# Optimization experiments

Hardware: AMD Instinct MI355X
Metric: run time of the kernel (lower is better)

## Reference

```python
import jax, jax.numpy as jnp
import numpy as np

N, IN_DIM, HID, E = 2048, 128, 64, 32768
EPS = 1e-5  # torch BatchNorm1d / LayerNorm default eps


def setup_inputs() -> dict:
    key = jax.random.key(0)
    ks = jax.random.split(key, 12)
    s = 0.05
    return {
        "h": jax.random.normal(ks[0], (N, IN_DIM), jnp.float32),
        "local": jax.random.normal(ks[1], (N, IN_DIM), jnp.float32),
        "e": jax.random.normal(ks[2], (E, HID), jnp.float32),
        "src": jax.random.randint(ks[3], (E,), 0, N, jnp.int32),
        "dst": jax.random.randint(ks[4], (E,), 0, N, jnp.int32),
        "ln_w": jnp.ones((IN_DIM,), jnp.float32),
        "ln_b": jnp.zeros((IN_DIM,), jnp.float32),
        "conv_w": jax.random.normal(ks[5], (1, 2, 3), jnp.float32) * 0.3,
        "conv_b": jnp.zeros((1,), jnp.float32),
        "W1": jax.random.normal(ks[6], (IN_DIM, HID * HID), jnp.float32) * s,
        "b1": jnp.zeros((HID * HID,), jnp.float32),
        "Wp2": jax.random.normal(ks[7], (IN_DIM, HID), jnp.float32) * s,
        "bp2": jnp.zeros((HID,), jnp.float32),
        "W2": jax.random.normal(ks[8], (IN_DIM, HID), jnp.float32) * s,
        "b2": jnp.zeros((HID,), jnp.float32),
        "W3": jax.random.normal(ks[9], (HID, HID), jnp.float32) * s,
        "b3": jnp.zeros((HID,), jnp.float32),
        "bng_g": jnp.ones((HID,), jnp.float32),
        "bng_b": jnp.zeros((HID,), jnp.float32),
        "bnG_g": jnp.ones((HID,), jnp.float32),
        "bnG_b": jnp.zeros((HID,), jnp.float32),
        "bnL_g": jnp.ones((HID,), jnp.float32),
        "bnL_b": jnp.zeros((HID,), jnp.float32),
    }


def _bn_eval(x, g, b):
    # BatchNorm1d in eval mode, running_mean=0, running_var=1
    return x * (g / jnp.sqrt(1.0 + EPS)) + b


def _layernorm(x, w, b):
    mu = jnp.mean(x, axis=-1, keepdims=True)
    var = jnp.var(x, axis=-1, keepdims=True)
    return (x - mu) / jnp.sqrt(var + EPS) * w + b


def reference(h, local, e, src, dst, ln_w, ln_b, conv_w, conv_b,
              W1, b1, Wp2, bp2, W2, b2, W3, b3,
              bng_g, bng_b, bnG_g, bnG_b, bnL_g, bnL_b):
    # ---- local edge branch ----
    edge = jnp.stack([local[src], local[dst]], axis=1)  # [E, 2, in_dim]
    edge = _layernorm(edge, ln_w, ln_b)
    # Conv1d(2 -> 1, k=3, pad=1) over the in_dim axis
    lr_local = jax.lax.conv_general_dilated(
        edge, conv_w, window_strides=(1,), padding=[(1, 1)],
        dimension_numbers=("NCH", "OIH", "NCH"))[:, 0, :] + conv_b  # [E, in_dim]
    lr_local = jax.nn.relu(lr_local)  # dropout is identity in eval
    lr_local = lr_local @ W2 + b2  # [E, hid]

    # ---- global edge branch ----
    p1 = jax.nn.relu(h @ W1 + b1).reshape(h.shape[0], HID, HID)  # [N, hid(d), hid(k)]
    p2 = jax.nn.relu(h @ Wp2 + bp2)  # [N, hid(k)]
    # mm[i, j, d] = sum_k p1[i, d, k] * p2[j, k]; gather only needed edges
    lr_global = jnp.einsum("edk,ek->ed", p1[src], p2[dst])  # [E, hid]
    lr_global = _bn_eval(lr_global, bng_g, bng_b) @ W3 + b3
    lr_global = jax.nn.relu(_bn_eval(lr_global, bnG_g, bnG_b))

    lr_local = jax.nn.relu(_bn_eval(lr_local, bnL_g, bnL_b))
    return lr_local + lr_global + e
```

## Files before the change

kernel.cpp:

```cpp
#include <hip/hip_runtime.h>

#define N_NODES 2048
#define IN_DIM 128
#define HID 64
#define N_EDGES 32768
#define EPS 1e-5f
#define MAX_TILES 4608

typedef short short8 __attribute__((ext_vector_type(8)));
typedef float f32x4 __attribute__((ext_vector_type(4)));

__device__ __forceinline__ float relu_f(float x) { return fmaxf(x, 0.f); }

__device__ __forceinline__ unsigned short f2bf(float f) {
  unsigned int u = __float_as_uint(f);
  u = (u + 0x7fffu + ((u >> 16) & 1u)) >> 16;
  return (unsigned short)u;
}
__device__ __forceinline__ float bf2f(unsigned short h) {
  return __uint_as_float(((unsigned int)h) << 16);
}
__device__ __forceinline__ short8 pack8(const float* f) {
  short8 o;
  #pragma unroll
  for (int i = 0; i < 8; ++i) o[i] = (short)f2bf(f[i]);
  return o;
}

__global__ __launch_bounds__(256) void prep_hist(
    const float* __restrict__ h, const float* __restrict__ local,
    const float* __restrict__ ln_w, const float* __restrict__ ln_b,
    const float* __restrict__ Wp2, const float* __restrict__ bp2,
    const float* __restrict__ W1, const float* __restrict__ W2,
    const float* __restrict__ W3, const int* __restrict__ src,
    unsigned short* __restrict__ hb, unsigned short* __restrict__ lnlb,
    unsigned short* __restrict__ p2b, unsigned short* __restrict__ w1t,
    unsigned short* __restrict__ w2tb, unsigned short* __restrict__ w3tb,
    int* __restrict__ cnt, int* __restrict__ perm_padded)
{
  __shared__ __align__(16) union {
    struct { float tile[IN_DIM][65]; } tr;
    struct { float hs[4][IN_DIM]; } p2s;
  } S;
  const int b = blockIdx.x, t = threadIdx.x;
  const int w = t >> 6, l = t & 63;

  if (b < 128) {
    int base = b * 2048 + t * 8;
    float4 v0 = *(const float4*)(h + base);
    float4 v1 = *(const float4*)(h + base + 4);
    ushort4 o0, o1;
    o0.x = f2bf(v0.x); o0.y = f2bf(v0.y); o0.z = f2bf(v0.z); o0.w = f2bf(v0.w);
    o1.x = f2bf(v1.x); o1.y = f2bf(v1.y); o1.z = f2bf(v1.z); o1.w = f2bf(v1.w);
    *(ushort4*)(hb + base) = o0;
    *(ushort4*)(hb + base + 4) = o1;
    int pbase = b * 576 + t;
    perm_padded[pbase] = -1;
    perm_padded[pbase + 256] = -1;
    if (t < 64) perm_padded[pbase + 512] = -1;
  } else if (b < 256) {
    int nb = b - 128;
    #pragma unroll
    for (int i = 0; i < 4; ++i) {
      int row = nb * 16 + w * 4 + i;
      const float* x = local + (size_t)row * IN_DIM;
      float x0 = x[l], x1 = x[l + 64];
      float s1 = x0 + x1, s2 = x0 * x0 + x1 * x1;
      #pragma unroll
      for (int off = 32; off > 0; off >>= 1) {
        s1 += __shfl_xor(s1, off);
        s2 += __shfl_xor(s2, off);
      }
      float mean = s1 * (1.f / IN_DIM);
      float var = s2 * (1.f / IN_DIM) - mean * mean;
      float rstd = rsqrtf(var + EPS);
      unsigned short* o = lnlb + (size_t)row * IN_DIM;
      o[l]      = f2bf((x0 - mean) * rstd * ln_w[l] + ln_b[l]);
      o[l + 64] = f2bf((x1 - mean) * rstd * ln_w[l + 64] + ln_b[l + 64]);
    }
    if (b == 128) {
      for (int i = t; i < IN_DIM * HID; i += 256) {
        int x = i >> 6, j = i & 63;
        w2tb[j * IN_DIM + x] = f2bf(W2[i]);
      }
    } else if (b == 129) {
      for (int i = t; i < HID * HID; i += 256) {
        int k = i >> 6, j = i & 63;
        w3tb[j * HID + k] = f2bf(W3[i]);
      }
    }
  } else if (b < 384) {
    int pb = b - 256;
    #pragma unroll
    for (int i = 0; i < 4; ++i) {
      int row = pb * 16 + w * 4 + i;
      S.p2s.hs[w][l] = h[(size_t)row * IN_DIM + l];
      S.p2s.hs[w][l + 64] = h[(size_t)row * IN_DIM + 64 + l];
      float acc = bp2[l];
      #pragma unroll 8
      for (int m = 0; m < IN_DIM; ++m) acc += S.p2s.hs[w][m] * Wp2[m * HID + l];
      p2b[(size_t)row * HID + l] = f2bf(relu_f(acc));
    }
  } else if (b < 448) {
    int n0 = (b - 384) * 64;
    int tx = t & 63, ty = t >> 6;
    #pragma unroll
    for (int r = 0; r < 32; ++r) {
      int k = r * 4 + ty;
      S.tr.tile[k][tx] = W1[(size_t)k * 4096 + n0 + tx];
    }
    __syncthreads();
    int j = t >> 2, kb = (t & 3) * 32;
    #pragma unroll
    for (int c = 0; c < 8; ++c) {
      ushort4 o;
      o.x = f2bf(S.tr.tile[kb + c * 4 + 0][j]);
      o.y = f2bf(S.tr.tile[kb + c * 4 + 1][j]);
      o.z = f2bf(S.tr.tile[kb + c * 4 + 2][j]);
      o.w = f2bf(S.tr.tile[kb + c * 4 + 3][j]);
      *(ushort4*)&w1t[(size_t)(n0 + j) * 128 + kb + c * 4] = o;
    }
  } else {
    int e0 = (b - 448) * 512 + t;
    atomicAdd(&cnt[src[e0]], 1);
    atomicAdd(&cnt[src[e0 + 256]], 1);
  }
}

__global__ __launch_bounds__(256) void gemm_scan(
    const unsigned short* __restrict__ hb, const unsigned short* __restrict__ w1t,
    const float* __restrict__ b1, unsigned short* __restrict__ p1b,
    const int* __restrict__ src, const int* __restrict__ cnt,
    int* __restrict__ cursor, int* __restrict__ ptile,
    int* __restrict__ tile_src, int* __restrict__ perm_padded)
{
  __shared__ __align__(16) struct { int part[256]; int pt[N_NODES]; } S;
  const int b = blockIdx.x, t = threadIdx.x;
  const int w = t >> 6, l = t & 63;
  const int lr = l & 15, lq = l >> 4;

  if (b < 1024) {
    const int bm = (b & 31) * 64;
    const int bn = (b >> 5) * 128;
    const int m0 = bm + w * 16;
    f32x4 acc[8];
    #pragma unroll
    for (int ni = 0; ni < 8; ++ni) acc[ni] = (f32x4){0.f, 0.f, 0.f, 0.f};
    #pragma unroll
    for (int k0 = 0; k0 < 128; k0 += 32) {
      short8 bmf = *(const short8*)(hb + (size_t)(m0 + lr) * 128 + k0 + lq * 8);
      #pragma unroll
      for (int ni = 0; ni < 8; ++ni) {
        short8 a = *(const short8*)(w1t + (size_t)(bn + ni * 16 + lr) * 128 + k0 + lq * 8);
        acc[ni] = __builtin_amdgcn_mfma_f32_16x16x32_bf16(a, bmf, acc[ni], 0, 0, 0);
      }
    }
    const int m = m0 + lr;
    #pragma unroll
    for (int ni = 0; ni < 8; ++ni) {
      int n = bn + ni * 16 + lq * 4;
      float4 bv = *(const float4*)&b1[n];
      ushort4 o;
      o.x = f2bf(relu_f(acc[ni][0] + bv.x));
      o.y = f2bf(relu_f(acc[ni][1] + bv.y));
      o.z = f2bf(relu_f(acc[ni][2] + bv.z));
      o.w = f2bf(relu_f(acc[ni][3] + bv.w));
      *(ushort4*)&p1b[(size_t)m * 4096 + n] = o;
    }
  } else {
    int nb = b - 1024;
    int locT[8];
    int s2 = 0;
    #pragma unroll
    for (int i = 0; i < 8; ++i) {
      locT[i] = s2;
      s2 += (cnt[t * 8 + i] + 15) >> 4;
    }
    S.part[t] = s2;
    __syncthreads();
    for (int off = 1; off < 256; off <<= 1) {
      int v = (t >= off) ? S.part[t - off] : 0;
      __syncthreads();
      S.part[t] += v;
      __syncthreads();
    }
    int base2 = (t == 0) ? 0 : S.part[t - 1];
    #pragma unroll
    for (int i = 0; i < 8; ++i) S.pt[t * 8 + i] = base2 + locT[i];
    if (nb == 0) {
      #pragma unroll
      for (int i = 0; i < 8; ++i) ptile[t * 8 + i] = base2 + locT[i];
      if (t == 255) ptile[N_NODES] = S.part[255];
    }
    __syncthreads();
    if (t < 16) {
      int node = nb * 16 + t;
      int base = S.pt[node];
      int nt = (cnt[node] + 15) >> 4;
      for (int k = 0; k < nt; ++k) tile_src[base + k] = node;
    }
    int e = nb * 256 + t;
    int s = src[e];
    int r = atomicAdd(&cursor[s], 1);
    perm_padded[S.pt[s] * 16 + r] = e;
  }
}

__global__ __launch_bounds__(256) void edge_mfma(
    const unsigned short* __restrict__ p1b, const unsigned short* __restrict__ p2b,
    const unsigned short* __restrict__ lnlb,
    const int* __restrict__ dst, const int* __restrict__ perm_padded,
    const int* __restrict__ tile_src, const int* __restrict__ ptile,
    const unsigned short* __restrict__ w2tb, const unsigned short* __restrict__ w3tb,
    const float* __restrict__ conv_w, const float* __restrict__ conv_b,
    const float* __restrict__ b2, const float* __restrict__ b3,
    const float* __restrict__ bng_g, const float* __restrict__ bng_b,
    const float* __restrict__ bnG_g, const float* __restrict__ bnG_b,
    const float* __restrict__ bnL_g, const float* __restrict__ bnL_b,
    const float* __restrict__ e_in, float* __restrict__ out)
{
  __shared__ float gs[4][16][68];
  __shared__ unsigned short ln1s[4][16][136];
  __shared__ unsigned short ln0s[4][136];

  const int t = threadIdx.x;
  const int w = t >> 6, l = t & 63;
  const int lr = l & 15, lq = l >> 4;
  const int n_tiles = ptile[N_NODES];
  const float rs = rsqrtf(1.f + EPS);

  float bngG[4], bngB[4], bnGG[4], bnGB[4], b3c[4], bnLG[4], bnLB[4], b2c[4];
  #pragma unroll
  for (int ni = 0; ni < 4; ++ni) {
    int col = ni * 16 + lr;
    bngG[ni] = bng_g[col] * rs; bngB[ni] = bng_b[col];
    bnGG[ni] = bnG_g[col] * rs; bnGB[ni] = bnG_b[col];
    bnLG[ni] = bnL_g[col] * rs; bnLB[ni] = bnL_b[col];
    b3c[ni] = b3[col]; b2c[ni] = b2[col];
  }
  const float cw0 = conv_w[0], cw1 = conv_w[1], cw2 = conv_w[2];
  const float cw3 = conv_w[3], cw4 = conv_w[4], cw5 = conv_w[5];
  const float cb = conv_b[0];

  for (int tile = blockIdx.x * 4 + w; tile < n_tiles; tile += gridDim.x * 4) {
    const int srcn = tile_src[tile];
    const int eidx = perm_padded[tile * 16 + lr];
    const int dn = (eidx >= 0) ? dst[eidx] : 0;

    {
      const unsigned short* r1 = lnlb + (size_t)dn * IN_DIM + lq * 32;
      #pragma unroll
      for (int c2 = 0; c2 < 4; ++c2)
        *(uint4*)&ln1s[w][lr][lq * 32 + c2 * 8] = *(const uint4*)(r1 + c2 * 8);
      if (l < 32)
        *(ushort4*)&ln0s[w][l * 4] = *(const ushort4*)(lnlb + (size_t)srcn * IN_DIM + l * 4);
    }

    const unsigned short* p2r = p2b + (size_t)dn * HID + lq * 8;
    short8 a0 = *(const short8*)(p2r);
    short8 a1 = *(const short8*)(p2r + 32);
    const unsigned short* pr = p1b + (size_t)srcn * 4096 + lr * 64 + lq * 8;
    f32x4 c[4];
    #pragma unroll
    for (int ni = 0; ni < 4; ++ni) {
      c[ni] = (f32x4){0.f, 0.f, 0.f, 0.f};
      short8 pb0 = *(const short8*)(pr + ni * 1024);
      short8 pb1 = *(const short8*)(pr + ni * 1024 + 32);
      c[ni] = __builtin_amdgcn_mfma_f32_16x16x32_bf16(a0, pb0, c[ni], 0, 0, 0);
      c[ni] = __builtin_amdgcn_mfma_f32_16x16x32_bf16(a1, pb1, c[ni], 0, 0, 0);
    }

    #pragma unroll
    for (int ni = 0; ni < 4; ++ni)
      #pragma unroll
      for (int r = 0; r < 4; ++r)
        gs[w][lq * 4 + r][ni * 16 + lr] = c[ni][r] * bngG[ni] + bngB[ni];
    asm volatile("s_waitcnt lgkmcnt(0)" ::: "memory");
    short8 ga0 = pack8(&gs[w][lr][lq * 8]);
    short8 ga1 = pack8(&gs[w][lr][32 + lq * 8]);

    const unsigned short* wr3 = w3tb + lr * HID + lq * 8;
    f32x4 u[4];
    #pragma unroll
    for (int ni = 0; ni < 4; ++ni) {
      u[ni] = (f32x4){0.f, 0.f, 0.f, 0.f};
      short8 wb0 = *(const short8*)(wr3 + ni * 1024);
      short8 wb1 = *(const short8*)(wr3 + ni * 1024 + 32);
      u[ni] = __builtin_amdgcn_mfma_f32_16x16x32_bf16(ga0, wb0, u[ni], 0, 0, 0);
      u[ni] = __builtin_amdgcn_mfma_f32_16x16x32_bf16(ga1, wb1, u[ni], 0, 0, 0);
    }

    asm volatile("s_waitcnt vmcnt(0) lgkmcnt(0)" ::: "memory");
    f32x4 v[4];
    #pragma unroll
    for (int ni = 0; ni < 4; ++ni) v[ni] = (f32x4){0.f, 0.f, 0.f, 0.f};
    #pragma unroll
    for (int ks = 0; ks < 4; ++ks) {
      short8 af;
      #pragma unroll
      for (int j = 0; j < 8; ++j) {
        int x = ks * 32 + lq * 8 + j;
        float am = (x > 0)   ? bf2f(ln0s[w][x - 1]) : 0.f;
        float az = bf2f(ln0s[w][x]);
        float ap = (x < 127) ? bf2f(ln0s[w][x + 1]) : 0.f;
        float bm = (x > 0)   ? bf2f(ln1s[w][lr][x - 1]) : 0.f;
        float bz = bf2f(ln1s[w][lr][x]);
        float bp = (x < 127) ? bf2f(ln1s[w][lr][x + 1]) : 0.f;
        float cv = relu_f(cw0 * am + cw1 * az + cw2 * ap +
                          cw3 * bm + cw4 * bz + cw5 * bp + cb);
        af[j] = (short)f2bf(cv);
      }
      #pragma unroll
      for (int ni = 0; ni < 4; ++ni) {
        short8 wb = *(const short8*)(w2tb + (size_t)(ni * 16 + lr) * IN_DIM + ks * 32 + lq * 8);
        v[ni] = __builtin_amdgcn_mfma_f32_16x16x32_bf16(af, wb, v[ni], 0, 0, 0);
      }
    }

    int er[4];
    #pragma unroll
    for (int r = 0; r < 4; ++r) er[r] = __shfl(eidx, lq * 4 + r);
    #pragma unroll
    for (int ni = 0; ni < 4; ++ni) {
      int col = ni * 16 + lr;
      #pragma unroll
      for (int r = 0; r < 4; ++r) {
        int e = er[r];
        if (e >= 0) {
          float vg = relu_f((u[ni][r] + b3c[ni]) * bnGG[ni] + bnGB[ni]);
          float vl = relu_f((v[ni][r] + b2c[ni]) * bnLG[ni] + bnLB[ni]);
          out[(size_t)e * HID + col] = vl + vg + e_in[(size_t)e * HID + col];
        }
      }
    }
  }
}

extern "C" void kernel_launch(void* const* d_in, const int* in_sizes, int n_in,
                              void* d_out, int out_size, void* d_ws, size_t ws_size,
                              hipStream_t stream) {
  const float* h      = (const float*)d_in[0];
  const float* local  = (const float*)d_in[1];
  const float* e_in   = (const float*)d_in[2];
  const int*   src    = (const int*)d_in[3];
  const int*   dst    = (const int*)d_in[4];
  const float* ln_w   = (const float*)d_in[5];
  const float* ln_b   = (const float*)d_in[6];
  const float* conv_w = (const float*)d_in[7];
  const float* conv_b = (const float*)d_in[8];
  const float* W1     = (const float*)d_in[9];
  const float* b1     = (const float*)d_in[10];
  const float* Wp2    = (const float*)d_in[11];
  const float* bp2    = (const float*)d_in[12];
  const float* W2     = (const float*)d_in[13];
  const float* b2     = (const float*)d_in[14];
  const float* W3     = (const float*)d_in[15];
  const float* b3     = (const float*)d_in[16];
  const float* bng_g  = (const float*)d_in[17];
  const float* bng_b  = (const float*)d_in[18];
  const float* bnG_g  = (const float*)d_in[19];
  const float* bnG_b  = (const float*)d_in[20];
  const float* bnL_g  = (const float*)d_in[21];
  const float* bnL_b  = (const float*)d_in[22];
  float* out = (float*)d_out;

  char* p = (char*)d_ws;
  unsigned short* p1b  = (unsigned short*)p; p += (size_t)N_NODES * HID * HID * 2;
  unsigned short* p2b  = (unsigned short*)p; p += (size_t)N_NODES * HID * 2;
  unsigned short* lnlb = (unsigned short*)p; p += (size_t)N_NODES * IN_DIM * 2;
  unsigned short* hb   = (unsigned short*)p; p += (size_t)N_NODES * IN_DIM * 2;
  unsigned short* w1t  = (unsigned short*)p; p += (size_t)4096 * 128 * 2;
  unsigned short* w2tb = (unsigned short*)p; p += (size_t)HID * IN_DIM * 2;
  unsigned short* w3tb = (unsigned short*)p; p += (size_t)HID * HID * 2;
  int* cnt    = (int*)p; p += N_NODES * 4;
  int* cursor = (int*)p; p += N_NODES * 4;
  int* ptile  = (int*)p; p += (N_NODES + 1) * 4;
  int* tile_src    = (int*)p; p += MAX_TILES * 4;
  int* perm_padded = (int*)p; p += (size_t)MAX_TILES * 16 * 4;

  hipMemsetAsync(cnt, 0, 2 * N_NODES * sizeof(int), stream);

  prep_hist<<<512, 256, 0, stream>>>(h, local, ln_w, ln_b, Wp2, bp2, W1, W2, W3, src,
                                     hb, lnlb, p2b, w1t, w2tb, w3tb, cnt, perm_padded);
  gemm_scan<<<1152, 256, 0, stream>>>(hb, w1t, b1, p1b, src, cnt, cursor,
                                      ptile, tile_src, perm_padded);
  edge_mfma<<<1024, 256, 0, stream>>>(p1b, p2b, lnlb, dst, perm_padded, tile_src, ptile,
                                      w2tb, w3tb, conv_w, conv_b, b2, b3,
                                      bng_g, bng_b, bnG_g, bnG_b, bnL_g, bnL_b, e_in, out);
}
```

Measured before the change: 173.0 us.

## Sort edges in single block with LDS histogram, drop memset, register conv stencil

Moves the per-source edge bucketing (histogram, scan, tile assignment, scatter) into one workgroup of the prep kernel using shared-memory atomics. This removes the global memset, the global atomic histogram and the scan blocks from the GEMM kernel, so p1_gemm becomes a pure GEMM. The edge kernel now computes the conv stencil straight from registers loaded from global memory instead of staging through LDS, which drops the LDS buffers and the full wait barrier. The risk is that the single sort block loops serially over all 32768 edges and may become the critical path of the prep kernel.

```diff
diff --git a/kernel.cpp b/kernel.cpp
--- a/kernel.cpp
+++ b/kernel.cpp
@@ -27,7 +27,7 @@
   return o;
 }
 
-__global__ __launch_bounds__(256) void prep_hist(
+__global__ __launch_bounds__(256) void prep_sort(
     const float* __restrict__ h, const float* __restrict__ local,
     const float* __restrict__ ln_w, const float* __restrict__ ln_b,
     const float* __restrict__ Wp2, const float* __restrict__ bp2,
@@ -36,11 +36,13 @@
     unsigned short* __restrict__ hb, unsigned short* __restrict__ lnlb,
     unsigned short* __restrict__ p2b, unsigned short* __restrict__ w1t,
     unsigned short* __restrict__ w2tb, unsigned short* __restrict__ w3tb,
-    int* __restrict__ cnt, int* __restrict__ perm_padded)
+    int* __restrict__ ntile, int* __restrict__ tile_src,
+    int* __restrict__ perm_padded)
 {
   __shared__ __align__(16) union {
     struct { float tile[IN_DIM][65]; } tr;
     struct { float hs[4][IN_DIM]; } p2s;
+    struct { int lh[N_NODES]; int cur[N_NODES]; int part[256]; } so;
   } S;
   const int b = blockIdx.x, t = threadIdx.x;
   const int w = t >> 6, l = t & 63;
@@ -54,10 +56,6 @@
     o1.x = f2bf(v1.x); o1.y = f2bf(v1.y); o1.z = f2bf(v1.z); o1.w = f2bf(v1.w);
     *(ushort4*)(hb + base) = o0;
     *(ushort4*)(hb + base + 4) = o1;
-    int pbase = b * 576 + t;
-    perm_padded[pbase] = -1;
-    perm_padded[pbase + 256] = -1;
-    if (t < 64) perm_padded[pbase + 512] = -1;
   } else if (b < 256) {
     int nb = b - 128;
     #pragma unroll
@@ -121,88 +119,83 @@
       *(ushort4*)&w1t[(size_t)(n0 + j) * 128 + kb + c * 4] = o;
     }
   } else {
-    int e0 = (b - 448) * 512 + t;
-    atomicAdd(&cnt[src[e0]], 1);
-    atomicAdd(&cnt[src[e0 + 256]], 1);
-  }
-}
-
-__global__ __launch_bounds__(256) void gemm_scan(
+    #pragma unroll
+    for (int i = 0; i < 8; ++i) S.so.lh[t * 8 + i] = 0;
+    __syncthreads();
+    for (int it = 0; it < 128; ++it)
+      atomicAdd(&S.so.lh[src[it * 256 + t]], 1);
+    __syncthreads();
+    int deg[8], locT[8];
+    int s2 = 0;
+    #pragma unroll
+    for (int i = 0; i < 8; ++i) {
+      deg[i] = S.so.lh[t * 8 + i];
+      locT[i] = s2;
+      s2 += (deg[i] + 15) >> 4;
+    }
+    S.so.part[t] = s2;
+    __syncthreads();
+    for (int off = 1; off < 256; off <<= 1) {
+      int v = (t >= off) ? S.so.part[t - off] : 0;
+      __syncthreads();
+      S.so.part[t] += v;
+      __syncthreads();
+    }
+    int base2 = (t == 0) ? 0 : S.so.part[t - 1];
+    if (t == 255) ntile[0] = S.so.part[255];
+    #pragma unroll
+    for (int i = 0; i < 8; ++i) {
+      int node = t * 8 + i;
+      int tb = base2 + locT[i];
+      int nt = (deg[i] + 15) >> 4;
+      S.so.cur[node] = tb * 16;
+      for (int k = 0; k < nt; ++k) tile_src[tb + k] = node;
+      for (int s = deg[i]; s < nt * 16; ++s) perm_padded[tb * 16 + s] = -1;
+    }
+    __syncthreads();
+    for (int it = 0; it < 128; ++it) {
+      int e = it * 256 + t;
+      int s = src[e];
+      int slot = atomicAdd(&S.so.cur[s], 1);
+      perm_padded[slot] = e;
+    }
+  }
+}
+
+__global__ __launch_bounds__(256) void p1_gemm(
     const unsigned short* __restrict__ hb, const unsigned short* __restrict__ w1t,
-    const float* __restrict__ b1, unsigned short* __restrict__ p1b,
-    const int* __restrict__ src, const int* __restrict__ cnt,
-    int* __restrict__ cursor, int* __restrict__ ptile,
-    int* __restrict__ tile_src, int* __restrict__ perm_padded)
+    const float* __restrict__ b1, unsigned short* __restrict__ p1b)
 {
-  __shared__ __align__(16) struct { int part[256]; int pt[N_NODES]; } S;
   const int b = blockIdx.x, t = threadIdx.x;
   const int w = t >> 6, l = t & 63;
   const int lr = l & 15, lq = l >> 4;
-
-  if (b < 1024) {
-    const int bm = (b & 31) * 64;
-    const int bn = (b >> 5) * 128;
-    const int m0 = bm + w * 16;
-    f32x4 acc[8];
-    #pragma unroll
-    for (int ni = 0; ni < 8; ++ni) acc[ni] = (f32x4){0.f, 0.f, 0.f, 0.f};
-    #pragma unroll
-    for (int k0 = 0; k0 < 128; k0 += 32) {
-      short8 bmf = *(const short8*)(hb + (size_t)(m0 + lr) * 128 + k0 + lq * 8);
-      #pragma unroll
-      for (int ni = 0; ni < 8; ++ni) {
-        short8 a = *(const short8*)(w1t + (size_t)(bn + ni * 16 + lr) * 128 + k0 + lq * 8);
-        acc[ni] = __builtin_amdgcn_mfma_f32_16x16x32_bf16(a, bmf, acc[ni], 0, 0, 0);
-      }
-    }
-    const int m = m0 + lr;
+  const int bm = (b & 31) * 64;
+  const int bn = (b >> 5) * 128;
+  const int m0 = bm + w * 16;
+
+  f32x4 acc[8];
+  #pragma unroll
+  for (int ni = 0; ni < 8; ++ni) acc[ni] = (f32x4){0.f, 0.f, 0.f, 0.f};
+  #pragma unroll
+  for (int k0 = 0; k0 < 128; k0 += 32) {
+    short8 bmf = *(const short8*)(hb + (size_t)(m0 + lr) * 128 + k0 + lq * 8);
     #pragma unroll
     for (int ni = 0; ni < 8; ++ni) {
-      int n = bn + ni * 16 + lq * 4;
-      float4 bv = *(const float4*)&b1[n];
-      ushort4 o;
-      o.x = f2bf(relu_f(acc[ni][0] + bv.x));
-      o.y = f2bf(relu_f(acc[ni][1] + bv.y));
-      o.z = f2bf(relu_f(acc[ni][2] + bv.z));
-      o.w = f2bf(relu_f(acc[ni][3] + bv.w));
-      *(ushort4*)&p1b[(size_t)m * 4096 + n] = o;
-    }
-  } else {
-    int nb = b - 1024;
-    int locT[8];
-    int s2 = 0;
-    #pragma unroll
-    for (int i = 0; i < 8; ++i) {
-      locT[i] = s2;
-      s2 += (cnt[t * 8 + i] + 15) >> 4;
-    }
-    S.part[t] = s2;
-    __syncthreads();
-    for (int off = 1; off < 256; off <<= 1) {
-      int v = (t >= off) ? S.part[t - off] : 0;
-      __syncthreads();
-      S.part[t] += v;
-      __syncthreads();
-    }
-    int base2 = (t == 0) ? 0 : S.part[t - 1];
-    #pragma unroll
-    for (int i = 0; i < 8; ++i) S.pt[t * 8 + i] = base2 + locT[i];
-    if (nb == 0) {
-      #pragma unroll
-      for (int i = 0; i < 8; ++i) ptile[t * 8 + i] = base2 + locT[i];
-      if (t == 255) ptile[N_NODES] = S.part[255];
-    }
-    __syncthreads();
-    if (t < 16) {
-      int node = nb * 16 + t;
-      int base = S.pt[node];
-      int nt = (cnt[node] + 15) >> 4;
-      for (int k = 0; k < nt; ++k) tile_src[base + k] = node;
-    }
-    int e = nb * 256 + t;
-    int s = src[e];
-    int r = atomicAdd(&cursor[s], 1);
-    perm_padded[S.pt[s] * 16 + r] = e;
+      short8 a = *(const short8*)(w1t + (size_t)(bn + ni * 16 + lr) * 128 + k0 + lq * 8);
+      acc[ni] = __builtin_amdgcn_mfma_f32_16x16x32_bf16(a, bmf, acc[ni], 0, 0, 0);
+    }
+  }
+  const int m = m0 + lr;
+  #pragma unroll
+  for (int ni = 0; ni < 8; ++ni) {
+    int n = bn + ni * 16 + lq * 4;
+    float4 bv = *(const float4*)&b1[n];
+    ushort4 o;
+    o.x = f2bf(relu_f(acc[ni][0] + bv.x));
+    o.y = f2bf(relu_f(acc[ni][1] + bv.y));
+    o.z = f2bf(relu_f(acc[ni][2] + bv.z));
+    o.w = f2bf(relu_f(acc[ni][3] + bv.w));
+    *(ushort4*)&p1b[(size_t)m * 4096 + n] = o;
   }
 }
 
@@ -210,7 +203,7 @@
     const unsigned short* __restrict__ p1b, const unsigned short* __restrict__ p2b,
     const unsigned short* __restrict__ lnlb,
     const int* __restrict__ dst, const int* __restrict__ perm_padded,
-    const int* __restrict__ tile_src, const int* __restrict__ ptile,
+    const int* __restrict__ tile_src, const int* __restrict__ ntile,
     const unsigned short* __restrict__ w2tb, const unsigned short* __restrict__ w3tb,
     const float* __restrict__ conv_w, const float* __restrict__ conv_b,
     const float* __restrict__ b2, const float* __restrict__ b3,
@@ -220,13 +213,11 @@
     const float* __restrict__ e_in, float* __restrict__ out)
 {
   __shared__ float gs[4][16][68];
-  __shared__ unsigned short ln1s[4][16][136];
-  __shared__ unsigned short ln0s[4][136];
 
   const int t = threadIdx.x;
   const int w = t >> 6, l = t & 63;
   const int lr = l & 15, lq = l >> 4;
-  const int n_tiles = ptile[N_NODES];
+  const int n_tiles = ntile[0];
   const float rs = rsqrtf(1.f + EPS);
 
   float bngG[4], bngB[4], bnGG[4], bnGB[4], b3c[4], bnLG[4], bnLB[4], b2c[4];
@@ -247,13 +238,52 @@
     const int eidx = perm_padded[tile * 16 + lr];
     const int dn = (eidx >= 0) ? dst[eidx] : 0;
 
-    {
-      const unsigned short* r1 = lnlb + (size_t)dn * IN_DIM + lq * 32;
-      #pragma unroll
-      for (int c2 = 0; c2 < 4; ++c2)
-        *(uint4*)&ln1s[w][lr][lq * 32 + c2 * 8] = *(const uint4*)(r1 + c2 * 8);
-      if (l < 32)
-        *(ushort4*)&ln0s[w][l * 4] = *(const ushort4*)(lnlb + (size_t)srcn * IN_DIM + l * 4);
+    const unsigned short* rowd = lnlb + (size_t)dn * IN_DIM;
+    const unsigned short* rows = lnlb + (size_t)srcn * IN_DIM;
+    short8 bch[4], ach[4];
+    #pragma unroll
+    for (int ks = 0; ks < 4; ++ks) {
+      bch[ks] = *(const short8*)(rowd + ks * 32 + lq * 8);
+      ach[ks] = *(const short8*)(rows + ks * 32 + lq * 8);
+    }
+    float aL[4], aR[4], bL[4], bR[4];
+    #pragma unroll
+    for (int ks = 0; ks < 4; ++ks) {
+      int kL = ks * 32 + lq * 8 - 1;
+      int kR = ks * 32 + lq * 8 + 8;
+      bool vL = (kL >= 0), vR = (kR < IN_DIM);
+      aL[ks] = vL ? bf2f(rows[kL]) : 0.f;
+      bL[ks] = vL ? bf2f(rowd[kL]) : 0.f;
+      aR[ks] = vR ? bf2f(rows[kR]) : 0.f;
+      bR[ks] = vR ? bf2f(rowd[kR]) : 0.f;
+    }
+    f32x4 v[4];
+    #pragma unroll
+    for (int ni = 0; ni < 4; ++ni) v[ni] = (f32x4){0.f, 0.f, 0.f, 0.f};
+    #pragma unroll
+    for (int ks = 0; ks < 4; ++ks) {
+      float A[8], B[8];
+      #pragma unroll
+      for (int j = 0; j < 8; ++j) {
+        A[j] = bf2f((unsigned short)ach[ks][j]);
+        B[j] = bf2f((unsigned short)bch[ks][j]);
+      }
+      short8 af;
+      #pragma unroll
+      for (int j = 0; j < 8; ++j) {
+        float am = j ? A[j - 1] : aL[ks];
+        float ap = (j < 7) ? A[j + 1] : aR[ks];
+        float bm = j ? B[j - 1] : bL[ks];
+        float bp = (j < 7) ? B[j + 1] : bR[ks];
+        float cv = relu_f(cw0 * am + cw1 * A[j] + cw2 * ap +
+                          cw3 * bm + cw4 * B[j] + cw5 * bp + cb);
+        af[j] = (short)f2bf(cv);
+      }
+      #pragma unroll
+      for (int ni = 0; ni < 4; ++ni) {
+        short8 wb = *(const short8*)(w2tb + (size_t)(ni * 16 + lr) * IN_DIM + ks * 32 + lq * 8);
+        v[ni] = __builtin_amdgcn_mfma_f32_16x16x32_bf16(af, wb, v[ni], 0, 0, 0);
+      }
     }
 
     const unsigned short* p2r = p2b + (size_t)dn * HID + lq * 8;
@@ -288,33 +318,6 @@
       short8 wb1 = *(const short8*)(wr3 + ni * 1024 + 32);
       u[ni] = __builtin_amdgcn_mfma_f32_16x16x32_bf16(ga0, wb0, u[ni], 0, 0, 0);
       u[ni] = __builtin_amdgcn_mfma_f32_16x16x32_bf16(ga1, wb1, u[ni], 0, 0, 0);
-    }
-
-    asm volatile("s_waitcnt vmcnt(0) lgkmcnt(0)" ::: "memory");
-    f32x4 v[4];
-    #pragma unroll
-    for (int ni = 0; ni < 4; ++ni) v[ni] = (f32x4){0.f, 0.f, 0.f, 0.f};
-    #pragma unroll
-    for (int ks = 0; ks < 4; ++ks) {
-      short8 af;
-      #pragma unroll
-      for (int j = 0; j < 8; ++j) {
-        int x = ks * 32 + lq * 8 + j;
-        float am = (x > 0)   ? bf2f(ln0s[w][x - 1]) : 0.f;
-        float az = bf2f(ln0s[w][x]);
-        float ap = (x < 127) ? bf2f(ln0s[w][x + 1]) : 0.f;
-        float bm = (x > 0)   ? bf2f(ln1s[w][lr][x - 1]) : 0.f;
-        float bz = bf2f(ln1s[w][lr][x]);
-        float bp = (x < 127) ? bf2f(ln1s[w][lr][x + 1]) : 0.f;
-        float cv = relu_f(cw0 * am + cw1 * az + cw2 * ap +
-                          cw3 * bm + cw4 * bz + cw5 * bp + cb);
-        af[j] = (short)f2bf(cv);
-      }
-      #pragma unroll
-      for (int ni = 0; ni < 4; ++ni) {
-        short8 wb = *(const short8*)(w2tb + (size_t)(ni * 16 + lr) * IN_DIM + ks * 32 + lq * 8);
-        v[ni] = __builtin_amdgcn_mfma_f32_16x16x32_bf16(af, wb, v[ni], 0, 0, 0);
-      }
     }
 
     int er[4];
@@ -372,19 +375,15 @@
   unsigned short* w1t  = (unsigned short*)p; p += (size_t)4096 * 128 * 2;
   unsigned short* w2tb = (unsigned short*)p; p += (size_t)HID * IN_DIM * 2;
   unsigned short* w3tb = (unsigned short*)p; p += (size_t)HID * HID * 2;
-  int* cnt    = (int*)p; p += N_NODES * 4;
-  int* cursor = (int*)p; p += N_NODES * 4;
-  int* ptile  = (int*)p; p += (N_NODES + 1) * 4;
-  int* tile_src    = (int*)p; p += MAX_TILES * 4;
+  int* ntile    = (int*)p; p += 16;
+  int* tile_src = (int*)p; p += MAX_TILES * 4;
   int* perm_padded = (int*)p; p += (size_t)MAX_TILES * 16 * 4;
 
-  hipMemsetAsync(cnt, 0, 2 * N_NODES * sizeof(int), stream);
-
-  prep_hist<<<512, 256, 0, stream>>>(h, local, ln_w, ln_b, Wp2, bp2, W1, W2, W3, src,
-                                     hb, lnlb, p2b, w1t, w2tb, w3tb, cnt, perm_padded);
-  gemm_scan<<<1152, 256, 0, stream>>>(hb, w1t, b1, p1b, src, cnt, cursor,
-                                      ptile, tile_src, perm_padded);
-  edge_mfma<<<1024, 256, 0, stream>>>(p1b, p2b, lnlb, dst, perm_padded, tile_src, ptile,
+  prep_sort<<<449, 256, 0, stream>>>(h, local, ln_w, ln_b, Wp2, bp2, W1, W2, W3, src,
+                                     hb, lnlb, p2b, w1t, w2tb, w3tb,
+                                     ntile, tile_src, perm_padded);
+  p1_gemm<<<1024, 256, 0, stream>>>(hb, w1t, b1, p1b);
+  edge_mfma<<<1024, 256, 0, stream>>>(p1b, p2b, lnlb, dst, perm_padded, tile_src, ntile,
                                       w2tb, w3tb, conv_w, conv_b, b2, b3,
                                       bng_g, bng_b, bnG_g, bnG_b, bnL_g, bnL_b, e_in, out);
 }
```

New measurement: 218.7 us. 1.26x slower.
